# Performance work log

Measured on AMD Instinct MI355X. Metric: run time of the kernel, lower is better.

Reference implementation:

```python
import jax, jax.numpy as jnp
import numpy as np

N = 8192      # agent_num
F = 128       # feature dim
P = 16        # persona dim
E = 262144    # edges (N * avg_degree 32)


def setup_inputs() -> dict:
    key = jax.random.key(0)
    ks = jax.random.split(key, 10)
    return {
        "feature": jax.random.normal(ks[0], (N, F), dtype=jnp.float32),
        "next_feature": jax.random.normal(ks[1], (N, F), dtype=jnp.float32),
        "persona_t": jax.random.uniform(ks[2], (N, P), dtype=jnp.float32),
        "alpha": jax.random.normal(ks[3], (P,), dtype=jnp.float32),
        "beta": jax.random.normal(ks[4], (P,), dtype=jnp.float32),
        "gamma": jax.random.normal(ks[5], (P,), dtype=jnp.float32),
        "act_src": jax.random.randint(ks[6], (E,), 0, N, dtype=jnp.int32),
        "act_dst": jax.random.randint(ks[7], (E,), 0, N, dtype=jnp.int32),
        "edge_src": jax.random.randint(ks[8], (E,), 0, N, dtype=jnp.int32),
        "edge_dst": jax.random.randint(ks[9], (E,), 0, N, dtype=jnp.int32),
    }


def _row_l2_normalize(x):
    # norm_func: divide each row by its L2 norm (scatter-add of squares in torch)
    norms = jnp.sqrt(jnp.sum(x * x, axis=1, keepdims=True))
    return x / norms


def reference(feature, next_feature, persona_t, alpha, beta, gamma,
              act_src, act_dst, edge_src, edge_dst):
    n, f = feature.shape

    # ---- impact (gamma) path: adj_sim_self(next_action, old - new) ----
    diff = feature - next_feature                           # [N, F]
    # hadamard(adj, diff @ diff.T): only dot products on action edges
    impact_vals = jnp.sum(diff[act_src] * diff[act_dst], axis=1) / f   # [E]
    gamma_row = persona_t @ gamma                            # [N] persona-weighted gamma
    reward_impact = impact_vals * gamma_row[act_src]         # row-wise multiply

    # ---- similarity (alpha) path: adj_sim(next_action, norm(next_feature)) ----
    # step() normalizes next_feature, then adj_sim normalizes again (idempotent)
    nf = _row_l2_normalize(_row_l2_normalize(next_feature))  # [N, F]
    sim_vals = jnp.sum(nf[act_src] * nf[act_dst], axis=1)    # [E] cosine sims on edges
    alpha_row = persona_t @ alpha                            # [N]
    reward_sim = sim_vals * alpha_row[act_src]

    # ---- cost (beta) path: old edges (binary) * persona_beta broadcast over rows ----
    beta_row = persona_t @ beta                              # [N]
    reward_cost = beta_row[edge_src]                         # [E] (edge value = 1)

    # ---- reward = reward_sim - reward_cost + reward_impact on the union of supports ----
    reward = jnp.zeros((n, n), dtype=feature.dtype)
    reward = reward.at[act_src, act_dst].add(reward_sim + reward_impact)
    reward = reward.at[edge_src, edge_dst].add(-reward_cost)
    return reward
```

## Files before the change

kernel.cpp:

```cpp
#include <hip/hip_runtime.h>

#define N_AGENTS 8192
#define FDIM 128
#define PDIM 16
#define NEDGES 262144

__global__ void zero_out_k(float4* __restrict__ out, int n4) {
    int i = blockIdx.x * blockDim.x + threadIdx.x;
    int stride = gridDim.x * blockDim.x;
    float4 z = make_float4(0.f, 0.f, 0.f, 0.f);
    for (; i < n4; i += stride) out[i] = z;
}

__global__ void row_prep_k(const float* __restrict__ feature,
                           const float* __restrict__ next_feature,
                           const float* __restrict__ persona,
                           const float* __restrict__ alpha,
                           const float* __restrict__ beta,
                           const float* __restrict__ gamma,
                           float* __restrict__ diff,
                           float* __restrict__ nf,
                           float* __restrict__ arow,
                           float* __restrict__ brow,
                           float* __restrict__ grow) {
    int row  = (blockIdx.x * blockDim.x + threadIdx.x) >> 6;
    int lane = threadIdx.x & 63;
    if (row >= N_AGENTS) return;

    const float2* f2 = (const float2*)(feature      + (size_t)row * FDIM);
    const float2* n2 = (const float2*)(next_feature + (size_t)row * FDIM);
    float2 f  = f2[lane];
    float2 nx = n2[lane];

    float2 d = make_float2(f.x - nx.x, f.y - nx.y);
    ((float2*)(diff + (size_t)row * FDIM))[lane] = d;

    float ss = nx.x * nx.x + nx.y * nx.y;

    float pa = 0.f, pb = 0.f, pg = 0.f;
    if (lane < PDIM) {
        float p = persona[(size_t)row * PDIM + lane];
        pa = p * alpha[lane];
        pb = p * beta[lane];
        pg = p * gamma[lane];
    }

    #pragma unroll
    for (int off = 32; off > 0; off >>= 1) {
        ss += __shfl_xor(ss, off);
        pa += __shfl_xor(pa, off);
        pb += __shfl_xor(pb, off);
        pg += __shfl_xor(pg, off);
    }

    float inv = 1.0f / sqrtf(ss);
    ((float2*)(nf + (size_t)row * FDIM))[lane] = make_float2(nx.x * inv, nx.y * inv);

    if (lane == 0) {
        arow[row] = pa;
        brow[row] = pb;
        grow[row] = pg;
    }
}

__global__ void act_edges_k(const int* __restrict__ asrc,
                            const int* __restrict__ adst,
                            const float* __restrict__ diff,
                            const float* __restrict__ nf,
                            const float* __restrict__ arow,
                            const float* __restrict__ grow,
                            float* __restrict__ out) {
    int gid = blockIdx.x * blockDim.x + threadIdx.x;
    int e   = gid >> 4;
    int sub = gid & 15;
    if (e >= NEDGES) return;

    int s = asrc[e];
    int d = adst[e];

    const float4* ds = (const float4*)(diff + (size_t)s * FDIM);
    const float4* dd = (const float4*)(diff + (size_t)d * FDIM);
    const float4* ns = (const float4*)(nf   + (size_t)s * FDIM);
    const float4* nd = (const float4*)(nf   + (size_t)d * FDIM);

    float imp = 0.f, sim = 0.f;
    #pragma unroll
    for (int k = 0; k < 2; ++k) {
        int idx = sub + k * 16;
        float4 a = ds[idx], b = dd[idx];
        imp += a.x * b.x + a.y * b.y + a.z * b.z + a.w * b.w;
        float4 c = ns[idx], g = nd[idx];
        sim += c.x * g.x + c.y * g.y + c.z * g.z + c.w * g.w;
    }

    #pragma unroll
    for (int off = 8; off > 0; off >>= 1) {
        imp += __shfl_xor(imp, off, 16);
        sim += __shfl_xor(sim, off, 16);
    }

    if (sub == 0) {
        float val = sim * arow[s] + imp * (1.0f / FDIM) * grow[s];
        atomicAdd(out + (size_t)s * N_AGENTS + d, val);
    }
}

__global__ void cost_edges_k(const int* __restrict__ esrc,
                             const int* __restrict__ edst,
                             const float* __restrict__ brow,
                             float* __restrict__ out) {
    int e = blockIdx.x * blockDim.x + threadIdx.x;
    if (e >= NEDGES) return;
    int s = esrc[e];
    atomicAdd(out + (size_t)s * N_AGENTS + edst[e], -brow[s]);
}

extern "C" void kernel_launch(void* const* d_in, const int* in_sizes, int n_in,
                              void* d_out, int out_size, void* d_ws, size_t ws_size,
                              hipStream_t stream) {
    const float* feature      = (const float*)d_in[0];
    const float* next_feature = (const float*)d_in[1];
    const float* persona      = (const float*)d_in[2];
    const float* alpha        = (const float*)d_in[3];
    const float* beta         = (const float*)d_in[4];
    const float* gamma        = (const float*)d_in[5];
    const int*   act_src      = (const int*)d_in[6];
    const int*   act_dst      = (const int*)d_in[7];
    const int*   edge_src     = (const int*)d_in[8];
    const int*   edge_dst     = (const int*)d_in[9];

    float* out = (float*)d_out;

    float* ws   = (float*)d_ws;
    float* diff = ws;
    float* nf   = diff + (size_t)N_AGENTS * FDIM;
    float* arow = nf   + (size_t)N_AGENTS * FDIM;
    float* brow = arow + N_AGENTS;
    float* grow = brow + N_AGENTS;

    int n4 = (N_AGENTS * N_AGENTS) / 4;
    zero_out_k<<<4096, 256, 0, stream>>>((float4*)out, n4);

    row_prep_k<<<N_AGENTS / 4, 256, 0, stream>>>(
        feature, next_feature, persona, alpha, beta, gamma,
        diff, nf, arow, brow, grow);

    act_edges_k<<<(NEDGES * 16) / 256, 256, 0, stream>>>(
        act_src, act_dst, diff, nf, arow, grow, out);

    cost_edges_k<<<NEDGES / 256, 256, 0, stream>>>(
        edge_src, edge_dst, brow, out);
}
```

Before: 376.6 us.

## Store features in fp16 interleaved rows, overlap edge dots with output zeroing

Row prep now writes the normalized next_feature and the diff as fp16 into one interleaved 256-half row per agent, and folds the 1/F factor into a packed per-row scale. A fused kernel runs the edge dot products in one set of blocks while the other blocks zero the 256MB output with nontemporal stores, and writes per-edge values to a buffer. A single scatter kernel then does both atomic passes. Halving the gather bytes and hiding the dot-product work under the bandwidth-bound zeroing should help, but fp16 storage reduces precision of the dot products.

Result: slower. 402.2 us (+6.8%).

```diff
diff --git a/kernel.cpp b/kernel.cpp
--- a/kernel.cpp
+++ b/kernel.cpp
@@ -1,28 +1,27 @@
 #include <hip/hip_runtime.h>
+#include <hip/hip_fp16.h>
 
 #define N_AGENTS 8192
 #define FDIM 128
 #define PDIM 16
 #define NEDGES 262144
 
-__global__ void zero_out_k(float4* __restrict__ out, int n4) {
-    int i = blockIdx.x * blockDim.x + threadIdx.x;
-    int stride = gridDim.x * blockDim.x;
-    float4 z = make_float4(0.f, 0.f, 0.f, 0.f);
-    for (; i < n4; i += stride) out[i] = z;
-}
+#define EDGE_BLOCKS 512
+#define ZERO_BLOCKS 1536
+#define OUT4 ((size_t)N_AGENTS * N_AGENTS / 4)
 
-__global__ void row_prep_k(const float* __restrict__ feature,
-                           const float* __restrict__ next_feature,
-                           const float* __restrict__ persona,
-                           const float* __restrict__ alpha,
-                           const float* __restrict__ beta,
-                           const float* __restrict__ gamma,
-                           float* __restrict__ diff,
-                           float* __restrict__ nf,
-                           float* __restrict__ arow,
-                           float* __restrict__ brow,
-                           float* __restrict__ grow) {
+typedef float floatx4 __attribute__((ext_vector_type(4)));
+
+__global__ __launch_bounds__(256) void row_prep_k(
+        const float* __restrict__ feature,
+        const float* __restrict__ next_feature,
+        const float* __restrict__ persona,
+        const float* __restrict__ alpha,
+        const float* __restrict__ beta,
+        const float* __restrict__ gamma,
+        __half2* __restrict__ T2,
+        float2* __restrict__ scale,
+        float* __restrict__ brow) {
     int row  = (blockIdx.x * blockDim.x + threadIdx.x) >> 6;
     int lane = threadIdx.x & 63;
     if (row >= N_AGENTS) return;
@@ -33,8 +32,6 @@
     float2 nx = n2[lane];
 
     float2 d = make_float2(f.x - nx.x, f.y - nx.y);
-    ((float2*)(diff + (size_t)row * FDIM))[lane] = d;
-
     float ss = nx.x * nx.x + nx.y * nx.y;
 
     float pa = 0.f, pb = 0.f, pg = 0.f;
@@ -54,65 +51,84 @@
     }
 
     float inv = 1.0f / sqrtf(ss);
-    ((float2*)(nf + (size_t)row * FDIM))[lane] = make_float2(nx.x * inv, nx.y * inv);
+    __half2* trow = T2 + (size_t)row * 128;
+    trow[lane]      = __float22half2_rn(make_float2(nx.x * inv, nx.y * inv));
+    trow[64 + lane] = __float22half2_rn(d);
 
     if (lane == 0) {
-        arow[row] = pa;
-        brow[row] = pb;
-        grow[row] = pg;
+        scale[row] = make_float2(pa, pg * (1.0f / FDIM));
+        brow[row]  = pb;
     }
 }
 
-__global__ void act_edges_k(const int* __restrict__ asrc,
-                            const int* __restrict__ adst,
-                            const float* __restrict__ diff,
-                            const float* __restrict__ nf,
-                            const float* __restrict__ arow,
-                            const float* __restrict__ grow,
-                            float* __restrict__ out) {
-    int gid = blockIdx.x * blockDim.x + threadIdx.x;
-    int e   = gid >> 4;
-    int sub = gid & 15;
-    if (e >= NEDGES) return;
+__device__ inline float dot8(float4 a, float4 b) {
+    const __half2* ha = (const __half2*)&a;
+    const __half2* hb = (const __half2*)&b;
+    float s = 0.f;
+    #pragma unroll
+    for (int j = 0; j < 4; ++j) {
+        float2 fa = __half22float2(ha[j]);
+        float2 fb = __half22float2(hb[j]);
+        s += fa.x * fb.x + fa.y * fb.y;
+    }
+    return s;
+}
 
-    int s = asrc[e];
-    int d = adst[e];
-
-    const float4* ds = (const float4*)(diff + (size_t)s * FDIM);
-    const float4* dd = (const float4*)(diff + (size_t)d * FDIM);
-    const float4* ns = (const float4*)(nf   + (size_t)s * FDIM);
-    const float4* nd = (const float4*)(nf   + (size_t)d * FDIM);
-
-    float imp = 0.f, sim = 0.f;
-    #pragma unroll
-    for (int k = 0; k < 2; ++k) {
-        int idx = sub + k * 16;
-        float4 a = ds[idx], b = dd[idx];
-        imp += a.x * b.x + a.y * b.y + a.z * b.z + a.w * b.w;
-        float4 c = ns[idx], g = nd[idx];
-        sim += c.x * g.x + c.y * g.y + c.z * g.z + c.w * g.w;
-    }
-
-    #pragma unroll
-    for (int off = 8; off > 0; off >>= 1) {
-        imp += __shfl_xor(imp, off, 16);
-        sim += __shfl_xor(sim, off, 16);
-    }
-
-    if (sub == 0) {
-        float val = sim * arow[s] + imp * (1.0f / FDIM) * grow[s];
-        atomicAdd(out + (size_t)s * N_AGENTS + d, val);
+__global__ __launch_bounds__(256) void fused_k(
+        const int* __restrict__ asrc,
+        const int* __restrict__ adst,
+        const __half* __restrict__ T,
+        const float2* __restrict__ scale,
+        float* __restrict__ vals,
+        floatx4* __restrict__ out4) {
+    int b = blockIdx.x;
+    if (b < EDGE_BLOCKS) {
+        int lane16 = threadIdx.x & 15;
+        int e      = (b * 256 + (int)threadIdx.x) >> 4;
+        const int estride = (EDGE_BLOCKS * 256) >> 4;
+        for (; e < NEDGES; e += estride) {
+            int s = asrc[e];
+            int d = adst[e];
+            const float4* ts = (const float4*)(T + (size_t)s * 256);
+            const float4* td = (const float4*)(T + (size_t)d * 256);
+            int i0 = lane16 * 2;
+            float acc = dot8(ts[i0], td[i0]) + dot8(ts[i0 + 1], td[i0 + 1]);
+            acc += __shfl_xor(acc, 1, 16);
+            acc += __shfl_xor(acc, 2, 16);
+            acc += __shfl_xor(acc, 4, 16);
+            float other = __shfl_xor(acc, 8, 16);
+            if (lane16 == 0) {
+                float2 sc = scale[s];
+                vals[e] = acc * sc.x + other * sc.y;
+            }
+        }
+    } else {
+        int zb = b - EDGE_BLOCKS;
+        size_t i = (size_t)zb * 256 + threadIdx.x;
+        const size_t stride = (size_t)ZERO_BLOCKS * 256;
+        floatx4 z = (floatx4)0.f;
+        for (; i < OUT4; i += stride)
+            __builtin_nontemporal_store(z, &out4[i]);
     }
 }
 
-__global__ void cost_edges_k(const int* __restrict__ esrc,
-                             const int* __restrict__ edst,
-                             const float* __restrict__ brow,
-                             float* __restrict__ out) {
-    int e = blockIdx.x * blockDim.x + threadIdx.x;
-    if (e >= NEDGES) return;
-    int s = esrc[e];
-    atomicAdd(out + (size_t)s * N_AGENTS + edst[e], -brow[s]);
+__global__ __launch_bounds__(256) void scatter_k(
+        const int* __restrict__ asrc,
+        const int* __restrict__ adst,
+        const int* __restrict__ esrc,
+        const int* __restrict__ edst,
+        const float* __restrict__ vals,
+        const float* __restrict__ brow,
+        float* __restrict__ out) {
+    int gid = blockIdx.x * blockDim.x + threadIdx.x;
+    if (gid < NEDGES) {
+        int s = asrc[gid];
+        atomicAdd(out + (size_t)s * N_AGENTS + adst[gid], vals[gid]);
+    } else {
+        int e = gid - NEDGES;
+        int s = esrc[e];
+        atomicAdd(out + (size_t)s * N_AGENTS + edst[e], -brow[s]);
+    }
 }
 
 extern "C" void kernel_launch(void* const* d_in, const int* in_sizes, int n_in,
@@ -131,23 +147,19 @@
 
     float* out = (float*)d_out;
 
-    float* ws   = (float*)d_ws;
-    float* diff = ws;
-    float* nf   = diff + (size_t)N_AGENTS * FDIM;
-    float* arow = nf   + (size_t)N_AGENTS * FDIM;
-    float* brow = arow + N_AGENTS;
-    float* grow = brow + N_AGENTS;
-
-    int n4 = (N_AGENTS * N_AGENTS) / 4;
-    zero_out_k<<<4096, 256, 0, stream>>>((float4*)out, n4);
+    char* ws = (char*)d_ws;
+    __half* T     = (__half*)ws;
+    float2* scale = (float2*)(ws + (size_t)N_AGENTS * 256 * sizeof(__half));
+    float*  brow  = (float*)((char*)scale + (size_t)N_AGENTS * sizeof(float2));
+    float*  vals  = (float*)((char*)brow  + (size_t)N_AGENTS * sizeof(float));
 
     row_prep_k<<<N_AGENTS / 4, 256, 0, stream>>>(
         feature, next_feature, persona, alpha, beta, gamma,
-        diff, nf, arow, brow, grow);
+        (__half2*)T, scale, brow);
 
-    act_edges_k<<<(NEDGES * 16) / 256, 256, 0, stream>>>(
-        act_src, act_dst, diff, nf, arow, grow, out);
+    fused_k<<<EDGE_BLOCKS + ZERO_BLOCKS, 256, 0, stream>>>(
+        act_src, act_dst, T, scale, vals, (floatx4*)out);
 
-    cost_edges_k<<<NEDGES / 256, 256, 0, stream>>>(
-        edge_src, edge_dst, brow, out);
+    scatter_k<<<(2 * NEDGES) / 256, 256, 0, stream>>>(
+        act_src, act_dst, edge_src, edge_dst, vals, brow, out);
 }
```
